# Kernel optimization log

Hardware: AMD Instinct MI355X
Metric: run time of the kernel (lower is better)

Reference implementation:

```python
import jax, jax.numpy as jnp
import numpy as np

D = 1024
H = 16
HD = D // H
B = 2
T = 2048


def setup_inputs() -> dict:
    key = jax.random.key(0)
    ks = jax.random.split(key, 5)
    x = jax.random.normal(ks[0], (B, T, D), dtype=jnp.float32)
    # PyTorch SDPA bool-mask semantics: True = attend. Causal lower-triangular.
    attn_mask = jnp.tril(jnp.ones((T, T), dtype=bool))
    w_qkv = jax.random.normal(ks[1], (3 * D, D), dtype=jnp.float32) * (1.0 / np.sqrt(D))
    b_qkv = jax.random.normal(ks[2], (3 * D,), dtype=jnp.float32) * 0.02
    w_proj = jax.random.normal(ks[3], (D, D), dtype=jnp.float32) * (1.0 / np.sqrt(D))
    b_proj = jax.random.normal(ks[4], (D,), dtype=jnp.float32) * 0.02
    return {"x": x, "attn_mask": attn_mask, "w_qkv": w_qkv, "b_qkv": b_qkv,
            "w_proj": w_proj, "b_proj": b_proj}


def reference(x, attn_mask, w_qkv, b_qkv, w_proj, b_proj):
    b, t, d = x.shape
    # fused QKV projection (torch Linear: y = x @ W.T + b)
    qkv = jnp.einsum('btd,ed->bte', x, w_qkv) + b_qkv  # [B,T,3D]
    q, k, v = jnp.split(qkv, 3, axis=-1)
    # [B,T,D] -> [B,H,T,hd]
    def heads(z):
        return z.reshape(b, t, H, HD).transpose(0, 2, 1, 3)
    q, k, v = heads(q), heads(k), heads(v)
    scale = 1.0 / jnp.sqrt(jnp.asarray(HD, dtype=x.dtype))
    scores = jnp.einsum('bhqd,bhkd->bhqk', q, k) * scale  # [B,H,T,T]
    neg_inf = jnp.asarray(jnp.finfo(x.dtype).min, dtype=x.dtype)
    scores = jnp.where(attn_mask, scores, neg_inf)
    attn = jax.nn.softmax(scores, axis=-1)
    y = jnp.einsum('bhqk,bhkd->bhqd', attn, v)  # [B,H,T,hd]
    y = y.transpose(0, 2, 1, 3).reshape(b, t, d)
    y = jnp.einsum('btd,ed->bte', y, w_proj) + b_proj
    return y
```

## Files before the change

### kernel.cpp

```cpp
#include <hip/hip_runtime.h>
#include <hip/hip_bf16.h>
#include <math.h>

#define D_MODEL 1024
#define NHEAD   16
#define HDIM    64
#define BATCH   2
#define SEQ     2048
#define MTOT    (BATCH * SEQ)

typedef unsigned short u16;
typedef unsigned int u32;
typedef short short8 __attribute__((ext_vector_type(8)));
typedef float floatx4 __attribute__((ext_vector_type(4)));

#define LOG2E 1.44269504088896340736f

#if __has_builtin(__builtin_amdgcn_exp2f)
#define EXP2(x) __builtin_amdgcn_exp2f(x)
#else
#define EXP2(x) exp2f(x)
#endif

static __device__ __forceinline__ u16 f2b(float f) {
  union { __hip_bfloat16 h; u16 u; } cv;
  cv.h = __float2bfloat16(f);
  return cv.u;
}

typedef const __attribute__((address_space(1))) unsigned int guint;
typedef __attribute__((address_space(3))) unsigned int luint;
static __device__ __forceinline__ void gl_lds16(const u16* g, u16* l) {
  __builtin_amdgcn_global_load_lds((guint*)g, (luint*)l, 16, 0, 0);
}

__global__ __launch_bounds__(256) void cast3_f2b(
    const float* __restrict__ a, u16* __restrict__ ao, int na,
    const float* __restrict__ b, u16* __restrict__ bo, int nb,
    const float* __restrict__ c, u16* __restrict__ co) {
  int i = (blockIdx.x * 256 + threadIdx.x) * 4;
  const float* src;
  u16* dst;
  if (i < na) {
    src = a + i;
    dst = ao + i;
  } else if (i < na + nb) {
    src = b + (i - na);
    dst = bo + (i - na);
  } else {
    src = c + (i - na - nb);
    dst = co + (i - na - nb);
  }
  float4 v = *(const float4*)src;
  ushort4 o;
  o.x = f2b(v.x);
  o.y = f2b(v.y);
  o.z = f2b(v.z);
  o.w = f2b(v.w);
  *(ushort4*)dst = o;
}

template <int MODE, int AR>
__global__ __launch_bounds__(256) void gemm_bt_bf16(
    const u16* __restrict__ A, const u16* __restrict__ Bm,
    const float* __restrict__ bias, u16* __restrict__ Cq, u16* __restrict__ Ck,
    u16* __restrict__ Cvt, float* __restrict__ Cf, int M, int N, int K) {
  constexpr int MI = AR / 32;
  constexpr int SMREQ = 2 * (AR + 128) * 32;
  constexpr int SM = (MODE == 0) ? (SMREQ > 17408 ? SMREQ : 17408) : SMREQ;
  __shared__ u16 smem[SM];
  u16(*As)[AR][32] = (u16(*)[AR][32])smem;
  u16(*Bs)[128][32] = (u16(*)[128][32])(smem + 2 * AR * 32);

  const int tid = threadIdx.x;
  const int lane = tid & 63;
  const int wave = tid >> 6;
  const int wm = (wave >> 1) * (AR / 2);
  const int wn = (wave & 1) * 64;
  const int quad = lane >> 4;
  const int l15 = lane & 15;
  const int m0 = blockIdx.y * AR;
  const int n0 = blockIdx.x * 128;

  const int srow = wave * 16 + (lane >> 2);
  const int k8 = (lane & 3) * 8;

  const u16* gA0 = A + (size_t)(m0 + srow) * K + k8;
  const u16* gA1 = A + (size_t)(m0 + srow + 64) * K + k8;
  const u16* gB0 = Bm + (size_t)(n0 + srow) * K + k8;
  const u16* gB1 = Bm + (size_t)(n0 + srow + 64) * K + k8;

  floatx4 acc[MI][4];
#pragma unroll
  for (int i = 0; i < MI; ++i)
#pragma unroll
    for (int j = 0; j < 4; ++j)
#pragma unroll
      for (int e = 0; e < 4; ++e) acc[i][j][e] = 0.0f;

  gl_lds16(gA0, &As[0][srow][k8]);
  if (AR == 128) gl_lds16(gA1, &As[0][srow + 64][k8]);
  gl_lds16(gB0, &Bs[0][srow][k8]);
  gl_lds16(gB1, &Bs[0][srow + 64][k8]);

  const int niter = K / 32;
  for (int kt = 0; kt < niter; ++kt) {
    const int cur = kt & 1;
    __syncthreads();
    if (kt + 1 < niter) {
      const int k0n = (kt + 1) * 32;
      gl_lds16(gA0 + k0n, &As[cur ^ 1][srow][k8]);
      if (AR == 128) gl_lds16(gA1 + k0n, &As[cur ^ 1][srow + 64][k8]);
      gl_lds16(gB0 + k0n, &Bs[cur ^ 1][srow][k8]);
      gl_lds16(gB1 + k0n, &Bs[cur ^ 1][srow + 64][k8]);
    }
    short8 af[MI], bf[4];
#pragma unroll
    for (int i = 0; i < MI; ++i)
      af[i] = *(const short8*)&As[cur][wm + i * 16 + l15][quad * 8];
#pragma unroll
    for (int j = 0; j < 4; ++j)
      bf[j] = *(const short8*)&Bs[cur][wn + j * 16 + l15][quad * 8];
#pragma unroll
    for (int i = 0; i < MI; ++i)
#pragma unroll
      for (int j = 0; j < 4; ++j)
        acc[i][j] = __builtin_amdgcn_mfma_f32_16x16x32_bf16(af[i], bf[j],
                                                            acc[i][j], 0, 0, 0);
  }

  if (MODE == 0) {
    const int nbase = n0 + wn;
    const int sel = nbase >> 10;
    const int h = (nbase >> 6) & (NHEAD - 1);
    if (sel == 2) {
#pragma unroll
      for (int j = 0; j < 4; ++j) {
        const int n = nbase + j * 16 + l15;
        const float bv = bias[n];
        const int d = n & (HDIM - 1);
#pragma unroll
        for (int i = 0; i < MI; ++i) {
          const int mb = m0 + wm + i * 16 + quad * 4;
          const int b = mb >> 11;
          const int t = mb & (SEQ - 1);
          ushort4 o4;
          o4.x = f2b(acc[i][j][0] + bv);
          o4.y = f2b(acc[i][j][1] + bv);
          o4.z = f2b(acc[i][j][2] + bv);
          o4.w = f2b(acc[i][j][3] + bv);
          *(ushort4*)(Cvt + ((size_t)(b * NHEAD + h) * HDIM + d) * SEQ + t) = o4;
        }
      }
    } else {
      u16* dst = (sel == 0) ? Cq : Ck;
      __syncthreads();
      u16(*Ct)[68] = (u16(*)[68])(smem + wave * 4352);
#pragma unroll
      for (int j = 0; j < 4; ++j) {
        const float bv = bias[nbase + j * 16 + l15];
#pragma unroll
        for (int i = 0; i < MI; ++i)
#pragma unroll
          for (int r = 0; r < 4; ++r)
            Ct[i * 16 + quad * 4 + r][j * 16 + l15] = f2b(acc[i][j][r] + bv);
      }
      const int mb0 = m0 + wm;
      const int b = mb0 >> 11;
      const int t0 = mb0 & (SEQ - 1);
      u16* rowbase = dst + ((size_t)(b * NHEAD + h) * SEQ + t0) * HDIM;
      const int tr = lane >> 3;
      const int d8 = (lane & 7) * 8;
#pragma unroll
      for (int p = 0; p < 8; ++p) {
        const int row = p * 8 + tr;
        *(short8*)(rowbase + (size_t)row * HDIM + d8) =
            *(const short8*)&Ct[row][d8];
      }
    }
  } else {
#pragma unroll
    for (int j = 0; j < 4; ++j) {
      const int n = n0 + wn + j * 16 + l15;
      const float bv = bias[n];
#pragma unroll
      for (int i = 0; i < MI; ++i) {
        const int mb = m0 + wm + i * 16 + quad * 4;
#pragma unroll
        for (int r = 0; r < 4; ++r)
          Cf[(size_t)(mb + r) * N + n] = acc[i][j][r] + bv;
      }
    }
  }
}

__global__ __launch_bounds__(256) void flash_mfma(const u16* __restrict__ Qg,
                                                  const u16* __restrict__ Kg,
                                                  const u16* __restrict__ Vtg,
                                                  u16* __restrict__ Yb) {
  __shared__ u16 Ks[2][64][76];
  __shared__ u16 Vt[2][80][76];
  __shared__ u16 Pb[64][76];

  const int tid = threadIdx.x;
  const int lane = tid & 63;
  const int wave = tid >> 6;
  const int wrow = wave * 16;
  const int quad = lane >> 4;
  const int l15 = lane & 15;
  const int bh = blockIdx.y;
  const int b = bh >> 4;
  const int h = bh & (NHEAD - 1);

  const u16* Qp = Qg + (size_t)bh * SEQ * HDIM;
  const u16* Kp = Kg + (size_t)bh * SEQ * HDIM;
  const u16* Vp = Vtg + (size_t)bh * HDIM * SEQ;

  const int srow = tid >> 2;
  const int sc = (tid & 3) * 16;

  const float scale2 = 0.125f * LOG2E;

#pragma unroll
  for (int bufi = 0; bufi < 2; ++bufi)
    for (int idx = tid; idx < 16 * 38; idx += 256) {
      const int row = 64 + idx / 38;
      const int c2 = (idx % 38) * 2;
      *(u32*)&Vt[bufi][row][c2] = (row == 64 && c2 < 64) ? 0x3F803F80u : 0u;
    }

#pragma unroll
  for (int phase = 0; phase < 2; ++phase) {
    const int qt = phase == 0 ? (16 + blockIdx.x) : (15 - blockIdx.x);
    const int q0 = qt * 64;

    __syncthreads();

    short8 aq[2];
    {
      const u16* qrow = Qp + (size_t)(q0 + wrow + l15) * HDIM + quad * 8;
      aq[0] = *(const short8*)qrow;
      aq[1] = *(const short8*)(qrow + 32);
    }

    floatx4 o[5];
#pragma unroll
    for (int c = 0; c < 5; ++c)
#pragma unroll
      for (int e = 0; e < 4; ++e) o[c][e] = 0.0f;

    const int nkt = qt + 1;
    short8 kv0 = *(const short8*)(Kp + (size_t)srow * HDIM + sc);
    short8 kv1 = *(const short8*)(Kp + (size_t)srow * HDIM + sc + 8);
    short8 vv0 = *(const short8*)(Vp + (size_t)srow * SEQ + sc);
    short8 vv1 = *(const short8*)(Vp + (size_t)srow * SEQ + sc + 8);

    for (int kt = 0; kt < nkt; ++kt) {
      const int k0 = kt * 64;
      const int buf = kt & 1;
      *(short8*)&Ks[buf][srow][sc] = kv0;
      *(short8*)&Ks[buf][srow][sc + 8] = kv1;
      *(short8*)&Vt[buf][srow][sc] = vv0;
      *(short8*)&Vt[buf][srow][sc + 8] = vv1;
      __syncthreads();
      if (kt + 1 < nkt) {
        const u16* kp = Kp + (size_t)(k0 + 64 + srow) * HDIM + sc;
        const u16* vp = Vp + (size_t)srow * SEQ + k0 + 64 + sc;
        kv0 = *(const short8*)kp;
        kv1 = *(const short8*)(kp + 8);
        vv0 = *(const short8*)vp;
        vv1 = *(const short8*)(vp + 8);
      }

      short8 bk[4][2];
#pragma unroll
      for (int c = 0; c < 4; ++c)
#pragma unroll
        for (int kk = 0; kk < 2; ++kk)
          bk[c][kk] =
              *(const short8*)&Ks[buf][c * 16 + l15][kk * 32 + quad * 8];

      floatx4 s[4];
#pragma unroll
      for (int c = 0; c < 4; ++c) {
#pragma unroll
        for (int e = 0; e < 4; ++e) s[c][e] = 0.0f;
        s[c] = __builtin_amdgcn_mfma_f32_16x16x32_bf16(aq[0], bk[c][0], s[c],
                                                       0, 0, 0);
        s[c] = __builtin_amdgcn_mfma_f32_16x16x32_bf16(aq[1], bk[c][1], s[c],
                                                       0, 0, 0);
      }

      const bool msk = (kt == nkt - 1);
      const int prow = wrow + quad * 4;
#pragma unroll
      for (int c = 0; c < 4; ++c)
#pragma unroll
        for (int r = 0; r < 4; ++r) {
          float v = s[c][r] * scale2;
          if (msk) {
            const int row = q0 + prow + r;
            const int col = k0 + c * 16 + l15;
            if (col > row) v = -INFINITY;
          }
          Pb[prow + r][c * 16 + l15] = f2b(EXP2(v));
        }

      short8 ap[2];
#pragma unroll
      for (int kk = 0; kk < 2; ++kk)
        ap[kk] = *(const short8*)&Pb[wrow + l15][kk * 32 + quad * 8];
#pragma unroll
      for (int c = 0; c < 5; ++c) {
        short8 bv0 = *(const short8*)&Vt[buf][c * 16 + l15][quad * 8];
        short8 bv1 = *(const short8*)&Vt[buf][c * 16 + l15][32 + quad * 8];
        o[c] = __builtin_amdgcn_mfma_f32_16x16x32_bf16(ap[0], bv0, o[c], 0, 0,
                                                       0);
        o[c] = __builtin_amdgcn_mfma_f32_16x16x32_bf16(ap[1], bv1, o[c], 0, 0,
                                                       0);
      }
    }

#pragma unroll
    for (int r = 0; r < 4; ++r) {
      const float lr = __shfl(o[4][r], lane & 48);
      const float inv = 1.0f / lr;
      const int t = q0 + wrow + quad * 4 + r;
#pragma unroll
      for (int c = 0; c < 4; ++c)
        Yb[((size_t)b * SEQ + t) * D_MODEL + h * HDIM + c * 16 + l15] =
            f2b(o[c][r] * inv);
    }
  }
}

extern "C" void kernel_launch(void* const* d_in, const int* in_sizes, int n_in,
                              void* d_out, int out_size, void* d_ws,
                              size_t ws_size, hipStream_t stream) {
  const float* x = (const float*)d_in[0];
  const float* w_qkv = (const float*)d_in[2];
  const float* b_qkv = (const float*)d_in[3];
  const float* w_proj = (const float*)d_in[4];
  const float* b_proj = (const float*)d_in[5];
  float* out = (float*)d_out;

  const size_t nx = (size_t)MTOT * D_MODEL;
  const size_t nwq = (size_t)3 * D_MODEL * D_MODEL;
  const size_t nwp = (size_t)D_MODEL * D_MODEL;
  const size_t nqkv = (size_t)BATCH * NHEAD * SEQ * HDIM;

  u16* xb = (u16*)d_ws;
  u16* wqb = xb + nx;
  u16* wpb = wqb + nwq;
  u16* qb = wpb + nwp;
  u16* kb = qb + nqkv;
  u16* vtb = kb + nqkv;
  u16* yb = vtb + nqkv;

  cast3_f2b<<<dim3((nx + nwq + nwp) / 1024), dim3(256), 0, stream>>>(
      x, xb, (int)nx, w_qkv, wqb, (int)nwq, w_proj, wpb);

  gemm_bt_bf16<0, 128><<<dim3(24, 32), dim3(256), 0, stream>>>(
      xb, wqb, b_qkv, qb, kb, vtb, nullptr, MTOT, 3 * D_MODEL, D_MODEL);
  flash_mfma<<<dim3(16, BATCH * NHEAD), dim3(256), 0, stream>>>(qb, kb, vtb,
                                                                yb);
  gemm_bt_bf16<1, 64><<<dim3(8, 64), dim3(256), 0, stream>>>(
      yb, wpb, b_proj, nullptr, nullptr, nullptr, out, MTOT, D_MODEL, D_MODEL);
}
```

Measured before the change: 188.2 us.

## Split flash grid per query tile, use ones-fragment rowsum, K64 proj GEMM

```diff
diff --git a/kernel.cpp b/kernel.cpp
--- a/kernel.cpp
+++ b/kernel.cpp
@@ -60,26 +60,22 @@
   *(ushort4*)dst = o;
 }
 
-template <int MODE, int AR>
-__global__ __launch_bounds__(256) void gemm_bt_bf16(
+__global__ __launch_bounds__(256) void gemm_qkv(
     const u16* __restrict__ A, const u16* __restrict__ Bm,
     const float* __restrict__ bias, u16* __restrict__ Cq, u16* __restrict__ Ck,
-    u16* __restrict__ Cvt, float* __restrict__ Cf, int M, int N, int K) {
-  constexpr int MI = AR / 32;
-  constexpr int SMREQ = 2 * (AR + 128) * 32;
-  constexpr int SM = (MODE == 0) ? (SMREQ > 17408 ? SMREQ : 17408) : SMREQ;
-  __shared__ u16 smem[SM];
-  u16(*As)[AR][32] = (u16(*)[AR][32])smem;
-  u16(*Bs)[128][32] = (u16(*)[128][32])(smem + 2 * AR * 32);
+    u16* __restrict__ Cvt, int M, int N, int K) {
+  __shared__ u16 smem[17408];
+  u16(*As)[128][32] = (u16(*)[128][32])smem;
+  u16(*Bs)[128][32] = (u16(*)[128][32])(smem + 8192);
 
   const int tid = threadIdx.x;
   const int lane = tid & 63;
   const int wave = tid >> 6;
-  const int wm = (wave >> 1) * (AR / 2);
+  const int wm = (wave >> 1) * 64;
   const int wn = (wave & 1) * 64;
   const int quad = lane >> 4;
   const int l15 = lane & 15;
-  const int m0 = blockIdx.y * AR;
+  const int m0 = blockIdx.y * 128;
   const int n0 = blockIdx.x * 128;
 
   const int srow = wave * 16 + (lane >> 2);
@@ -90,16 +86,16 @@
   const u16* gB0 = Bm + (size_t)(n0 + srow) * K + k8;
   const u16* gB1 = Bm + (size_t)(n0 + srow + 64) * K + k8;
 
-  floatx4 acc[MI][4];
-#pragma unroll
-  for (int i = 0; i < MI; ++i)
+  floatx4 acc[4][4];
+#pragma unroll
+  for (int i = 0; i < 4; ++i)
 #pragma unroll
     for (int j = 0; j < 4; ++j)
 #pragma unroll
       for (int e = 0; e < 4; ++e) acc[i][j][e] = 0.0f;
 
   gl_lds16(gA0, &As[0][srow][k8]);
-  if (AR == 128) gl_lds16(gA1, &As[0][srow + 64][k8]);
+  gl_lds16(gA1, &As[0][srow + 64][k8]);
   gl_lds16(gB0, &Bs[0][srow][k8]);
   gl_lds16(gB1, &Bs[0][srow + 64][k8]);
 
@@ -110,86 +106,164 @@
     if (kt + 1 < niter) {
       const int k0n = (kt + 1) * 32;
       gl_lds16(gA0 + k0n, &As[cur ^ 1][srow][k8]);
-      if (AR == 128) gl_lds16(gA1 + k0n, &As[cur ^ 1][srow + 64][k8]);
+      gl_lds16(gA1 + k0n, &As[cur ^ 1][srow + 64][k8]);
       gl_lds16(gB0 + k0n, &Bs[cur ^ 1][srow][k8]);
       gl_lds16(gB1 + k0n, &Bs[cur ^ 1][srow + 64][k8]);
     }
-    short8 af[MI], bf[4];
-#pragma unroll
-    for (int i = 0; i < MI; ++i)
+    short8 af[4], bf[4];
+#pragma unroll
+    for (int i = 0; i < 4; ++i)
       af[i] = *(const short8*)&As[cur][wm + i * 16 + l15][quad * 8];
 #pragma unroll
     for (int j = 0; j < 4; ++j)
       bf[j] = *(const short8*)&Bs[cur][wn + j * 16 + l15][quad * 8];
 #pragma unroll
-    for (int i = 0; i < MI; ++i)
+    for (int i = 0; i < 4; ++i)
 #pragma unroll
       for (int j = 0; j < 4; ++j)
         acc[i][j] = __builtin_amdgcn_mfma_f32_16x16x32_bf16(af[i], bf[j],
                                                             acc[i][j], 0, 0, 0);
   }
 
-  if (MODE == 0) {
-    const int nbase = n0 + wn;
-    const int sel = nbase >> 10;
-    const int h = (nbase >> 6) & (NHEAD - 1);
-    if (sel == 2) {
+  const int nbase = n0 + wn;
+  const int sel = nbase >> 10;
+  const int h = (nbase >> 6) & (NHEAD - 1);
+  if (sel == 2) {
+#pragma unroll
+    for (int j = 0; j < 4; ++j) {
+      const int n = nbase + j * 16 + l15;
+      const float bv = bias[n];
+      const int d = n & (HDIM - 1);
+#pragma unroll
+      for (int i = 0; i < 4; ++i) {
+        const int mb = m0 + wm + i * 16 + quad * 4;
+        const int b = mb >> 11;
+        const int t = mb & (SEQ - 1);
+        ushort4 o4;
+        o4.x = f2b(acc[i][j][0] + bv);
+        o4.y = f2b(acc[i][j][1] + bv);
+        o4.z = f2b(acc[i][j][2] + bv);
+        o4.w = f2b(acc[i][j][3] + bv);
+        *(ushort4*)(Cvt + ((size_t)(b * NHEAD + h) * HDIM + d) * SEQ + t) = o4;
+      }
+    }
+  } else {
+    u16* dst = (sel == 0) ? Cq : Ck;
+    __syncthreads();
+    u16(*Ct)[68] = (u16(*)[68])(smem + wave * 4352);
+#pragma unroll
+    for (int j = 0; j < 4; ++j) {
+      const float bv = bias[nbase + j * 16 + l15];
+#pragma unroll
+      for (int i = 0; i < 4; ++i)
+#pragma unroll
+        for (int r = 0; r < 4; ++r)
+          Ct[i * 16 + quad * 4 + r][j * 16 + l15] = f2b(acc[i][j][r] + bv);
+    }
+    const int mb0 = m0 + wm;
+    const int b = mb0 >> 11;
+    const int t0 = mb0 & (SEQ - 1);
+    u16* rowbase = dst + ((size_t)(b * NHEAD + h) * SEQ + t0) * HDIM;
+    const int tr = lane >> 3;
+    const int d8 = (lane & 7) * 8;
+#pragma unroll
+    for (int p = 0; p < 8; ++p) {
+      const int row = p * 8 + tr;
+      *(short8*)(rowbase + (size_t)row * HDIM + d8) =
+          *(const short8*)&Ct[row][d8];
+    }
+  }
+}
+
+__global__ __launch_bounds__(256) void gemm_proj_k64(
+    const u16* __restrict__ A, const u16* __restrict__ Bm,
+    const float* __restrict__ bias, float* __restrict__ Cf, int M, int N,
+    int K) {
+  __shared__ u16 As[2][64][64];
+  __shared__ u16 Bs[2][128][64];
+
+  const int tid = threadIdx.x;
+  const int lane = tid & 63;
+  const int wave = tid >> 6;
+  const int wm = (wave >> 1) * 32;
+  const int wn = (wave & 1) * 64;
+  const int quad = lane >> 4;
+  const int l15 = lane & 15;
+  const int m0 = blockIdx.y * 64;
+  const int n0 = blockIdx.x * 128;
+
+  const int srow = wave * 8 + (lane >> 3);
+  const int k8 = (lane & 7) * 8;
+
+  const u16* gA0 = A + (size_t)(m0 + srow) * K + k8;
+  const u16* gA1 = A + (size_t)(m0 + srow + 32) * K + k8;
+  const u16* gB0 = Bm + (size_t)(n0 + srow) * K + k8;
+  const u16* gB1 = Bm + (size_t)(n0 + srow + 32) * K + k8;
+  const u16* gB2 = Bm + (size_t)(n0 + srow + 64) * K + k8;
+  const u16* gB3 = Bm + (size_t)(n0 + srow + 96) * K + k8;
+
+  floatx4 acc[2][4];
+#pragma unroll
+  for (int i = 0; i < 2; ++i)
+#pragma unroll
+    for (int j = 0; j < 4; ++j)
+#pragma unroll
+      for (int e = 0; e < 4; ++e) acc[i][j][e] = 0.0f;
+
+  gl_lds16(gA0, &As[0][srow][k8]);
+  gl_lds16(gA1, &As[0][srow + 32][k8]);
+  gl_lds16(gB0, &Bs[0][srow][k8]);
+  gl_lds16(gB1, &Bs[0][srow + 32][k8]);
+  gl_lds16(gB2, &Bs[0][srow + 64][k8]);
+  gl_lds16(gB3, &Bs[0][srow + 96][k8]);
+
+  const int niter = K / 64;
+  for (int kt = 0; kt < niter; ++kt) {
+    const int cur = kt & 1;
+    __syncthreads();
+    if (kt + 1 < niter) {
+      const int k0n = (kt + 1) * 64;
+      gl_lds16(gA0 + k0n, &As[cur ^ 1][srow][k8]);
+      gl_lds16(gA1 + k0n, &As[cur ^ 1][srow + 32][k8]);
+      gl_lds16(gB0 + k0n, &Bs[cur ^ 1][srow][k8]);
+      gl_lds16(gB1 + k0n, &Bs[cur ^ 1][srow + 32][k8]);
+      gl_lds16(gB2 + k0n, &Bs[cur ^ 1][srow + 64][k8]);
+      gl_lds16(gB3 + k0n, &Bs[cur ^ 1][srow + 96][k8]);
+    }
+    short8 af[2][2], bf[4][2];
+#pragma unroll
+    for (int i = 0; i < 2; ++i)
+#pragma unroll
+      for (int kk = 0; kk < 2; ++kk)
+        af[i][kk] =
+            *(const short8*)&As[cur][wm + i * 16 + l15][kk * 32 + quad * 8];
+#pragma unroll
+    for (int j = 0; j < 4; ++j)
+#pragma unroll
+      for (int kk = 0; kk < 2; ++kk)
+        bf[j][kk] =
+            *(const short8*)&Bs[cur][wn + j * 16 + l15][kk * 32 + quad * 8];
+#pragma unroll
+    for (int i = 0; i < 2; ++i)
 #pragma unroll
       for (int j = 0; j < 4; ++j) {
-        const int n = nbase + j * 16 + l15;
-        const float bv = bias[n];
-        const int d = n & (HDIM - 1);
-#pragma unroll
-        for (int i = 0; i < MI; ++i) {
-          const int mb = m0 + wm + i * 16 + quad * 4;
-          const int b = mb >> 11;
-          const int t = mb & (SEQ - 1);
-          ushort4 o4;
-          o4.x = f2b(acc[i][j][0] + bv);
-          o4.y = f2b(acc[i][j][1] + bv);
-          o4.z = f2b(acc[i][j][2] + bv);
-          o4.w = f2b(acc[i][j][3] + bv);
-          *(ushort4*)(Cvt + ((size_t)(b * NHEAD + h) * HDIM + d) * SEQ + t) = o4;
-        }
+        acc[i][j] = __builtin_amdgcn_mfma_f32_16x16x32_bf16(
+            af[i][0], bf[j][0], acc[i][j], 0, 0, 0);
+        acc[i][j] = __builtin_amdgcn_mfma_f32_16x16x32_bf16(
+            af[i][1], bf[j][1], acc[i][j], 0, 0, 0);
       }
-    } else {
-      u16* dst = (sel == 0) ? Cq : Ck;
-      __syncthreads();
-      u16(*Ct)[68] = (u16(*)[68])(smem + wave * 4352);
-#pragma unroll
-      for (int j = 0; j < 4; ++j) {
-        const float bv = bias[nbase + j * 16 + l15];
-#pragma unroll
-        for (int i = 0; i < MI; ++i)
-#pragma unroll
-          for (int r = 0; r < 4; ++r)
-            Ct[i * 16 + quad * 4 + r][j * 16 + l15] = f2b(acc[i][j][r] + bv);
-      }
-      const int mb0 = m0 + wm;
-      const int b = mb0 >> 11;
-      const int t0 = mb0 & (SEQ - 1);
-      u16* rowbase = dst + ((size_t)(b * NHEAD + h) * SEQ + t0) * HDIM;
-      const int tr = lane >> 3;
-      const int d8 = (lane & 7) * 8;
-#pragma unroll
-      for (int p = 0; p < 8; ++p) {
-        const int row = p * 8 + tr;
-        *(short8*)(rowbase + (size_t)row * HDIM + d8) =
-            *(const short8*)&Ct[row][d8];
-      }
-    }
-  } else {
-#pragma unroll
-    for (int j = 0; j < 4; ++j) {
-      const int n = n0 + wn + j * 16 + l15;
-      const float bv = bias[n];
-#pragma unroll
-      for (int i = 0; i < MI; ++i) {
-        const int mb = m0 + wm + i * 16 + quad * 4;
-#pragma unroll
-        for (int r = 0; r < 4; ++r)
-          Cf[(size_t)(mb + r) * N + n] = acc[i][j][r] + bv;
-      }
+  }
+
+#pragma unroll
+  for (int j = 0; j < 4; ++j) {
+    const int n = n0 + wn + j * 16 + l15;
+    const float bv = bias[n];
+#pragma unroll
+    for (int i = 0; i < 2; ++i) {
+      const int mb = m0 + wm + i * 16 + quad * 4;
+#pragma unroll
+      for (int r = 0; r < 4; ++r)
+        Cf[(size_t)(mb + r) * N + n] = acc[i][j][r] + bv;
     }
   }
 }
@@ -199,7 +273,7 @@
                                                   const u16* __restrict__ Vtg,
                                                   u16* __restrict__ Yb) {
   __shared__ u16 Ks[2][64][76];
-  __shared__ u16 Vt[2][80][76];
+  __shared__ u16 Vt[2][64][76];
   __shared__ u16 Pb[64][76];
 
   const int tid = threadIdx.x;
@@ -221,116 +295,113 @@
 
   const float scale2 = 0.125f * LOG2E;
 
-#pragma unroll
-  for (int bufi = 0; bufi < 2; ++bufi)
-    for (int idx = tid; idx < 16 * 38; idx += 256) {
-      const int row = 64 + idx / 38;
-      const int c2 = (idx % 38) * 2;
-      *(u32*)&Vt[bufi][row][c2] = (row == 64 && c2 < 64) ? 0x3F803F80u : 0u;
-    }
-
-#pragma unroll
-  for (int phase = 0; phase < 2; ++phase) {
-    const int qt = phase == 0 ? (16 + blockIdx.x) : (15 - blockIdx.x);
-    const int q0 = qt * 64;
-
+  const int qt = 31 - blockIdx.x;
+  const int q0 = qt * 64;
+
+  short8 onesf;
+  {
+    const short ov = (l15 == 0) ? (short)0x3F80 : (short)0;
+#pragma unroll
+    for (int e = 0; e < 8; ++e) onesf[e] = ov;
+  }
+
+  short8 aq[2];
+  {
+    const u16* qrow = Qp + (size_t)(q0 + wrow + l15) * HDIM + quad * 8;
+    aq[0] = *(const short8*)qrow;
+    aq[1] = *(const short8*)(qrow + 32);
+  }
+
+  floatx4 o[5];
+#pragma unroll
+  for (int c = 0; c < 5; ++c)
+#pragma unroll
+    for (int e = 0; e < 4; ++e) o[c][e] = 0.0f;
+
+  const int nkt = qt + 1;
+  short8 kv0 = *(const short8*)(Kp + (size_t)srow * HDIM + sc);
+  short8 kv1 = *(const short8*)(Kp + (size_t)srow * HDIM + sc + 8);
+  short8 vv0 = *(const short8*)(Vp + (size_t)srow * SEQ + sc);
+  short8 vv1 = *(const short8*)(Vp + (size_t)srow * SEQ + sc + 8);
+
+  for (int kt = 0; kt < nkt; ++kt) {
+    const int k0 = kt * 64;
+    const int buf = kt & 1;
+    *(short8*)&Ks[buf][srow][sc] = kv0;
+    *(short8*)&Ks[buf][srow][sc + 8] = kv1;
+    *(short8*)&Vt[buf][srow][sc] = vv0;
+    *(short8*)&Vt[buf][srow][sc + 8] = vv1;
     __syncthreads();
-
-    short8 aq[2];
-    {
-      const u16* qrow = Qp + (size_t)(q0 + wrow + l15) * HDIM + quad * 8;
-      aq[0] = *(const short8*)qrow;
-      aq[1] = *(const short8*)(qrow + 32);
-    }
-
-    floatx4 o[5];
-#pragma unroll
-    for (int c = 0; c < 5; ++c)
-#pragma unroll
-      for (int e = 0; e < 4; ++e) o[c][e] = 0.0f;
-
-    const int nkt = qt + 1;
-    short8 kv0 = *(const short8*)(Kp + (size_t)srow * HDIM + sc);
-    short8 kv1 = *(const short8*)(Kp + (size_t)srow * HDIM + sc + 8);
-    short8 vv0 = *(const short8*)(Vp + (size_t)srow * SEQ + sc);
-    short8 vv1 = *(const short8*)(Vp + (size_t)srow * SEQ + sc + 8);
-
-    for (int kt = 0; kt < nkt; ++kt) {
-      const int k0 = kt * 64;
-      const int buf = kt & 1;
-      *(short8*)&Ks[buf][srow][sc] = kv0;
-      *(short8*)&Ks[buf][srow][sc + 8] = kv1;
-      *(short8*)&Vt[buf][srow][sc] = vv0;
-      *(short8*)&Vt[buf][srow][sc + 8] = vv1;
-      __syncthreads();
-      if (kt + 1 < nkt) {
-        const u16* kp = Kp + (size_t)(k0 + 64 + srow) * HDIM + sc;
-        const u16* vp = Vp + (size_t)srow * SEQ + k0 + 64 + sc;
-        kv0 = *(const short8*)kp;
-        kv1 = *(const short8*)(kp + 8);
-        vv0 = *(const short8*)vp;
-        vv1 = *(const short8*)(vp + 8);
+    if (kt + 1 < nkt) {
+      const u16* kp = Kp + (size_t)(k0 + 64 + srow) * HDIM + sc;
+      const u16* vp = Vp + (size_t)srow * SEQ + k0 + 64 + sc;
+      kv0 = *(const short8*)kp;
+      kv1 = *(const short8*)(kp + 8);
+      vv0 = *(const short8*)vp;
+      vv1 = *(const short8*)(vp + 8);
+    }
+
+    short8 bk[4][2];
+#pragma unroll
+    for (int c = 0; c < 4; ++c)
+#pragma unroll
+      for (int kk = 0; kk < 2; ++kk)
+        bk[c][kk] = *(const short8*)&Ks[buf][c * 16 + l15][kk * 32 + quad * 8];
+
+    floatx4 s[4];
+#pragma unroll
+    for (int c = 0; c < 4; ++c) {
+#pragma unroll
+      for (int e = 0; e < 4; ++e) s[c][e] = 0.0f;
+      s[c] = __builtin_amdgcn_mfma_f32_16x16x32_bf16(aq[0], bk[c][0], s[c], 0,
+                                                     0, 0);
+      s[c] = __builtin_amdgcn_mfma_f32_16x16x32_bf16(aq[1], bk[c][1], s[c], 0,
+                                                     0, 0);
+    }
+
+    const bool msk = (kt == nkt - 1);
+    const int prow = wrow + quad * 4;
+#pragma unroll
+    for (int c = 0; c < 4; ++c)
+#pragma unroll
+      for (int r = 0; r < 4; ++r) {
+        float v = s[c][r] * scale2;
+        if (msk) {
+          const int row = q0 + prow + r;
+          const int col = k0 + c * 16 + l15;
+          if (col > row) v = -INFINITY;
+        }
+        Pb[prow + r][c * 16 + l15] = f2b(EXP2(v));
       }
 
-      short8 bk[4][2];
-#pragma unroll
-      for (int c = 0; c < 4; ++c)
-#pragma unroll
-        for (int kk = 0; kk < 2; ++kk)
-          bk[c][kk] =
-              *(const short8*)&Ks[buf][c * 16 + l15][kk * 32 + quad * 8];
-
-      floatx4 s[4];
-#pragma unroll
-      for (int c = 0; c < 4; ++c) {
-#pragma unroll
-        for (int e = 0; e < 4; ++e) s[c][e] = 0.0f;
-        s[c] = __builtin_amdgcn_mfma_f32_16x16x32_bf16(aq[0], bk[c][0], s[c],
-                                                       0, 0, 0);
-        s[c] = __builtin_amdgcn_mfma_f32_16x16x32_bf16(aq[1], bk[c][1], s[c],
-                                                       0, 0, 0);
-      }
-
-      const bool msk = (kt == nkt - 1);
-      const int prow = wrow + quad * 4;
-#pragma unroll
-      for (int c = 0; c < 4; ++c)
-#pragma unroll
-        for (int r = 0; r < 4; ++r) {
-          float v = s[c][r] * scale2;
-          if (msk) {
-            const int row = q0 + prow + r;
-            const int col = k0 + c * 16 + l15;
-            if (col > row) v = -INFINITY;
-          }
-          Pb[prow + r][c * 16 + l15] = f2b(EXP2(v));
-        }
-
-      short8 ap[2];
-#pragma unroll
-      for (int kk = 0; kk < 2; ++kk)
-        ap[kk] = *(const short8*)&Pb[wrow + l15][kk * 32 + quad * 8];
-#pragma unroll
-      for (int c = 0; c < 5; ++c) {
-        short8 bv0 = *(const short8*)&Vt[buf][c * 16 + l15][quad * 8];
-        short8 bv1 = *(const short8*)&Vt[buf][c * 16 + l15][32 + quad * 8];
-        o[c] = __builtin_amdgcn_mfma_f32_16x16x32_bf16(ap[0], bv0, o[c], 0, 0,
-                                                       0);
-        o[c] = __builtin_amdgcn_mfma_f32_16x16x32_bf16(ap[1], bv1, o[c], 0, 0,
-                                                       0);
-      }
-    }
-
-#pragma unroll
-    for (int r = 0; r < 4; ++r) {
-      const float lr = __shfl(o[4][r], lane & 48);
-      const float inv = 1.0f / lr;
-      const int t = q0 + wrow + quad * 4 + r;
-#pragma unroll
-      for (int c = 0; c < 4; ++c)
-        Yb[((size_t)b * SEQ + t) * D_MODEL + h * HDIM + c * 16 + l15] =
-            f2b(o[c][r] * inv);
-    }
+    short8 ap[2];
+#pragma unroll
+    for (int kk = 0; kk < 2; ++kk)
+      ap[kk] = *(const short8*)&Pb[wrow + l15][kk * 32 + quad * 8];
+#pragma unroll
+    for (int c = 0; c < 4; ++c) {
+      short8 bv0 = *(const short8*)&Vt[buf][c * 16 + l15][quad * 8];
+      short8 bv1 = *(const short8*)&Vt[buf][c * 16 + l15][32 + quad * 8];
+      o[c] = __builtin_amdgcn_mfma_f32_16x16x32_bf16(ap[0], bv0, o[c], 0, 0,
+                                                     0);
+      o[c] = __builtin_amdgcn_mfma_f32_16x16x32_bf16(ap[1], bv1, o[c], 0, 0,
+                                                     0);
+    }
+    o[4] = __builtin_amdgcn_mfma_f32_16x16x32_bf16(ap[0], onesf, o[4], 0, 0,
+                                                   0);
+    o[4] = __builtin_amdgcn_mfma_f32_16x16x32_bf16(ap[1], onesf, o[4], 0, 0,
+                                                   0);
+  }
+
+#pragma unroll
+  for (int r = 0; r < 4; ++r) {
+    const float lr = __shfl(o[4][r], lane & 48);
+    const float inv = 1.0f / lr;
+    const int t = q0 + wrow + quad * 4 + r;
+#pragma unroll
+    for (int c = 0; c < 4; ++c)
+      Yb[((size_t)b * SEQ + t) * D_MODEL + h * HDIM + c * 16 + l15] =
+          f2b(o[c][r] * inv);
   }
 }
 
@@ -360,10 +431,10 @@
   cast3_f2b<<<dim3((nx + nwq + nwp) / 1024), dim3(256), 0, stream>>>(
       x, xb, (int)nx, w_qkv, wqb, (int)nwq, w_proj, wpb);
 
-  gemm_bt_bf16<0, 128><<<dim3(24, 32), dim3(256), 0, stream>>>(
-      xb, wqb, b_qkv, qb, kb, vtb, nullptr, MTOT, 3 * D_MODEL, D_MODEL);
-  flash_mfma<<<dim3(16, BATCH * NHEAD), dim3(256), 0, stream>>>(qb, kb, vtb,
+  gemm_qkv<<<dim3(24, 32), dim3(256), 0, stream>>>(
+      xb, wqb, b_qkv, qb, kb, vtb, MTOT, 3 * D_MODEL, D_MODEL);
+  flash_mfma<<<dim3(32, BATCH * NHEAD), dim3(256), 0, stream>>>(qb, kb, vtb,
                                                                 yb);
-  gemm_bt_bf16<1, 64><<<dim3(8, 64), dim3(256), 0, stream>>>(
-      yb, wpb, b_proj, nullptr, nullptr, nullptr, out, MTOT, D_MODEL, D_MODEL);
-}
+  gemm_proj_k64<<<dim3(8, 64), dim3(256), 0, stream>>>(
+      yb, wpb, b_proj, out, MTOT, D_MODEL, D_MODEL);
+}
```

Measured after the change: 218.7 us. +16.2%, slower.
